# Kernel optimization log

Hardware: AMD Instinct MI355X
Metric: run time of the kernel (lower is better)

## Reference

```python
import jax, jax.numpy as jnp
import numpy as np

S, B, D = 4096, 4, 1024
APERTURE = 256
SCALE = 1.0 / np.sqrt(D)
EPS = 1e-6
NEG_INF = -jnp.inf


def _xavier(key, shape, gain=np.sqrt(2.0)):
    fan_in, fan_out = shape[1], shape[0]
    a = gain * np.sqrt(6.0 / (fan_in + fan_out))
    return jax.random.uniform(key, shape, jnp.float32, -a, a)


def setup_inputs() -> dict:
    key = jax.random.key(0)
    ks = jax.random.split(key, 8)
    return {
        "x": jax.random.normal(ks[0], (S, B, D), jnp.float32),
        "Wk": _xavier(ks[1], (D, D)),
        "Wq": _xavier(ks[2], (D, D)),
        "Wv": _xavier(ks[3], (D, D)),
        "Wp": _xavier(ks[4], (D, D)),
        "W1": _xavier(ks[5], (D, D)),
        "b1": jnp.full((D,), 0.1, jnp.float32),
        "W2": _xavier(ks[6], (1, D)),
        "b2": jnp.full((1,), 0.1, jnp.float32),
        "gamma": jnp.ones((D,), jnp.float32),
        "beta": jnp.zeros((D,), jnp.float32),
    }


def _layer_norm(y, gamma, beta):
    m = jnp.mean(y, axis=-1, keepdims=True)
    v = jnp.mean((y - m) ** 2, axis=-1, keepdims=True)
    return (y - m) * jax.lax.rsqrt(v + EPS) * gamma + beta


def reference(x, Wk, Wq, Wv, Wp, W1, b1, W2, b2, gamma, beta):
    # x: (S, B, D) -> (B, S, D)
    xb = jnp.transpose(x, (1, 0, 2))
    K = jnp.einsum('bsd,ed->bse', xb, Wk)
    Q = jnp.einsum('bsd,ed->bse', xb, Wq)
    V = jnp.einsum('bsd,ed->bse', xb, Wv)
    e = jnp.einsum('bqd,bkd->bqk', Q, K) * SCALE  # (B, S, S)
    # ignore_self: -inf on diagonal
    eye = jnp.eye(S, dtype=bool)
    e = jnp.where(eye[None, :, :], NEG_INF, e)
    # aperture mask: torch masks where tril(e,ap)*triu(e,-ap) == 0
    scope = jnp.tril(e, APERTURE) * jnp.triu(e, -APERTURE)
    e = jnp.where(scope == 0, NEG_INF, e)
    alpha = jax.nn.softmax(e, axis=2)  # dropout is identity at eval
    c = jnp.einsum('bqk,bkd->bqd', alpha, V)
    c = jnp.einsum('bqd,ed->bqe', c, Wp)
    y = c + xb
    y = _layer_norm(y, gamma, beta)
    y = jax.nn.relu(jnp.einsum('bsd,ed->bse', y, W1) + b1)
    y = _layer_norm(y, gamma, beta)
    y = jax.nn.sigmoid(jnp.einsum('bsd,ed->bse', y, W2) + b2)  # (B, S, 1)
    return jnp.transpose(y, (1, 0, 2))  # (S, B, 1)
```

## Files before the change

### kernel.cpp

```cpp
#include <hip/hip_runtime.h>
#include <stdint.h>
#include <math.h>

#define S_LEN 4096
#define BATCH 4
#define DIM   1024
#define AP    256
#define NBLK  32
#define BANDC 640
#define SCALE 0.03125f

typedef __attribute__((ext_vector_type(4))) float f32x4;
typedef __attribute__((ext_vector_type(8))) short bf16x8;

__device__ __forceinline__ ushort f2bf(float f) {
  union { float f; uint32_t u; } v; v.f = f;
  uint32_t r = v.u + 0x7FFFu + ((v.u >> 16) & 1u);
  return (ushort)(r >> 16);
}

__device__ __forceinline__ void gload16(const void* g, void* l) {
  __builtin_amdgcn_global_load_lds((const __attribute__((address_space(1))) void*)g,
                                   (__attribute__((address_space(3))) void*)l,
                                   16, 0, 0);
}

__device__ __forceinline__ float block_sum(float v, float* red) {
  #pragma unroll
  for (int o = 32; o > 0; o >>= 1) v += __shfl_xor(v, o, 64);
  const int w = threadIdx.x >> 6;
  if ((threadIdx.x & 63) == 0) red[w] = v;
  __syncthreads();
  v = red[0] + red[1] + red[2] + red[3];
  __syncthreads();
  return v;
}

__device__ __forceinline__ float block_max(float v, float* red) {
  #pragma unroll
  for (int o = 32; o > 0; o >>= 1) v = fmaxf(v, __shfl_xor(v, o, 64));
  const int w = threadIdx.x >> 6;
  if ((threadIdx.x & 63) == 0) red[w] = v;
  __syncthreads();
  v = fmaxf(fmaxf(red[0], red[1]), fmaxf(red[2], red[3]));
  __syncthreads();
  return v;
}

__device__ __forceinline__ void gemm256_core(
    const ushort* __restrict__ Ablk, int lda,
    const ushort* __restrict__ Bblk, int ldb,
    int K, ushort* __restrict__ lds,
    f32x4 acc[8][4])
{
  const int tid  = threadIdx.x;
  const int lane = tid & 63;
  const int wave = tid >> 6;
  const int wr = wave >> 2;
  const int wn = wave & 3;

  const int srow = tid >> 2;
  const int gseg = (tid & 3) ^ ((tid >> 3) & 3);
  const ushort* gA0 = Ablk + (size_t)srow * lda + gseg * 8;
  const ushort* gA1 = Ablk + (size_t)(srow + 128) * lda + gseg * 8;
  const ushort* gB0 = Bblk + (size_t)srow * ldb + gseg * 8;
  const ushort* gB1 = Bblk + (size_t)(srow + 128) * ldb + gseg * 8;
  const int stA = wave * 512;

  const int l15 = lane & 15;
  const int seg = (lane >> 4) ^ ((lane >> 1) & 3);
  const int roffA = (wr * 128 + l15) * 32 + seg * 8;
  const int roffB = (wn * 64  + l15) * 32 + seg * 8;

  const int NT = K >> 5;

  #pragma unroll
  for (int p = 0; p < 3; ++p) {
    ushort* buf = lds + p * 16384;
    const int k0 = p * 32;
    gload16(gA0 + k0, buf + stA);
    gload16(gA1 + k0, buf + 4096  + stA);
    gload16(gB0 + k0, buf + 8192  + stA);
    gload16(gB1 + k0, buf + 12288 + stA);
  }

  for (int t = 0; t < NT; ++t) {
    const int rem = NT - 1 - t;
    if (rem >= 2)      asm volatile("s_waitcnt vmcnt(8)" ::: "memory");
    else if (rem == 1) asm volatile("s_waitcnt vmcnt(4)" ::: "memory");
    else               asm volatile("s_waitcnt vmcnt(0)" ::: "memory");
    __builtin_amdgcn_s_barrier();

    if (t + 3 < NT) {
      ushort* buf = lds + ((t + 3) & 3) * 16384;
      const int k0 = (t + 3) * 32;
      gload16(gA0 + k0, buf + stA);
      gload16(gA1 + k0, buf + 4096  + stA);
      gload16(gB0 + k0, buf + 8192  + stA);
      gload16(gB1 + k0, buf + 12288 + stA);
    }

    const ushort* buf = lds + (t & 3) * 16384;
    bf16x8 af[4], af2[4], bfv[4];
    #pragma unroll
    for (int n = 0; n < 4; ++n) bfv[n] = *(const bf16x8*)(buf + 8192 + roffB + n * 512);
    #pragma unroll
    for (int m = 0; m < 4; ++m) af[m] = *(const bf16x8*)(buf + roffA + m * 512);
    #pragma unroll
    for (int m = 0; m < 4; ++m) af2[m] = *(const bf16x8*)(buf + roffA + (m + 4) * 512);

    __builtin_amdgcn_s_setprio(1);
    #pragma unroll
    for (int m = 0; m < 4; ++m)
      #pragma unroll
      for (int n = 0; n < 4; ++n)
        acc[m][n] = __builtin_amdgcn_mfma_f32_16x16x32_bf16(af[m], bfv[n], acc[m][n], 0, 0, 0);
    #pragma unroll
    for (int m = 0; m < 4; ++m)
      #pragma unroll
      for (int n = 0; n < 4; ++n)
        acc[m + 4][n] = __builtin_amdgcn_mfma_f32_16x16x32_bf16(af2[m], bfv[n], acc[m + 4][n], 0, 0, 0);
    __builtin_amdgcn_s_setprio(0);
    asm volatile("s_waitcnt lgkmcnt(0)" ::: "memory");
  }
}

#define ACC256_ZERO(acc) \
  _Pragma("unroll") for (int m_ = 0; m_ < 8; m_++) \
  _Pragma("unroll") for (int n_ = 0; n_ < 4; n_++) \
  _Pragma("unroll") for (int r_ = 0; r_ < 4; r_++) acc[m_][n_][r_] = 0.0f;

#define EPI256_BEGIN(acc) { \
  const int lane_ = threadIdx.x & 63; \
  const int wave_ = threadIdx.x >> 6; \
  const int wrb_ = (wave_ >> 2) * 128; \
  const int wnb_ = (wave_ & 3) * 64; \
  const int rb_ = (lane_ >> 4) << 2; \
  const int cb_ = lane_ & 15; \
  _Pragma("unroll") for (int m_ = 0; m_ < 8; m_++) \
  _Pragma("unroll") for (int n_ = 0; n_ < 4; n_++) \
  _Pragma("unroll") for (int r_ = 0; r_ < 4; r_++) { \
    const int rloc = wrb_ + m_ * 16 + rb_ + r_; \
    const int cloc = wnb_ + n_ * 16 + cb_; \
    const float aval = acc[m_][n_][r_];
#define EPI256_END() } }

__device__ __forceinline__ void gemm_core(
    const ushort* __restrict__ Ablk, int lda,
    const ushort* __restrict__ Bblk, int ldb,
    int k_begin, int k_end,
    ushort* __restrict__ lds,
    f32x4 acc[4][4])
{
  const int tid  = threadIdx.x;
  const int lane = tid & 63;
  const int wr = ((tid >> 7) & 1) * 64;
  const int wc = ((tid >> 6) & 1) * 64;
  const int lr = lane & 15;
  const int seg = (lane >> 4) ^ ((lane >> 1) & 3);

  const int srow = tid >> 2;
  const int gseg = (tid & 3) ^ ((tid >> 3) & 3);
  const ushort* gA0 = Ablk + (size_t)srow * lda + gseg * 8;
  const ushort* gA1 = Ablk + (size_t)(srow + 64) * lda + gseg * 8;
  const ushort* gB0 = Bblk + (size_t)srow * ldb + gseg * 8;
  const ushort* gB1 = Bblk + (size_t)(srow + 64) * ldb + gseg * 8;
  const int stA = (tid >> 6) * 512;

  const int NT = (k_end - k_begin) >> 5;

  gload16(gA0 + k_begin, lds + stA);
  gload16(gA1 + k_begin, lds + 2048 + stA);
  gload16(gB0 + k_begin, lds + 4096 + stA);
  gload16(gB1 + k_begin, lds + 6144 + stA);

  for (int t = 0; t < NT; ++t) {
    if (t + 1 < NT) {
      ushort* buf = lds + ((t + 1) & 1) * 8192;
      const int k0 = k_begin + (t + 1) * 32;
      gload16(gA0 + k0, buf + stA);
      gload16(gA1 + k0, buf + 2048 + stA);
      gload16(gB0 + k0, buf + 4096 + stA);
      gload16(gB1 + k0, buf + 6144 + stA);
      asm volatile("s_waitcnt vmcnt(4)" ::: "memory");
    } else {
      asm volatile("s_waitcnt vmcnt(0)" ::: "memory");
    }
    __builtin_amdgcn_s_barrier();

    const ushort* buf = lds + (t & 1) * 8192;
    bf16x8 af[4], bfv[4];
    #pragma unroll
    for (int m = 0; m < 4; m++)
      af[m] = *(const bf16x8*)(buf + (wr + m * 16 + lr) * 32 + seg * 8);
    #pragma unroll
    for (int n = 0; n < 4; n++)
      bfv[n] = *(const bf16x8*)(buf + 4096 + (wc + n * 16 + lr) * 32 + seg * 8);

    __builtin_amdgcn_s_setprio(1);
    #pragma unroll
    for (int m = 0; m < 4; m++)
      #pragma unroll
      for (int n = 0; n < 4; n++)
        acc[m][n] = __builtin_amdgcn_mfma_f32_16x16x32_bf16(af[m], bfv[n], acc[m][n], 0, 0, 0);
    __builtin_amdgcn_s_setprio(0);
    asm volatile("s_waitcnt lgkmcnt(0)" ::: "memory");
  }
}

#define ACC_ZERO(acc) \
  _Pragma("unroll") for (int m_ = 0; m_ < 4; m_++) \
  _Pragma("unroll") for (int n_ = 0; n_ < 4; n_++) \
  _Pragma("unroll") for (int r_ = 0; r_ < 4; r_++) acc[m_][n_][r_] = 0.0f;

#define EPI_BEGIN(acc) { \
  const int lane_ = threadIdx.x & 63; \
  const int wr_ = ((threadIdx.x >> 7) & 1) * 64; \
  const int wc_ = ((threadIdx.x >> 6) & 1) * 64; \
  const int rb_ = (lane_ >> 4) << 2; \
  const int cb_ = lane_ & 15; \
  _Pragma("unroll") for (int m_ = 0; m_ < 4; m_++) \
  _Pragma("unroll") for (int n_ = 0; n_ < 4; n_++) \
  _Pragma("unroll") for (int r_ = 0; r_ < 4; r_++) { \
    const int rloc = wr_ + m_ * 16 + rb_ + r_; \
    const int cloc = wc_ + n_ * 16 + cb_; \
    const float aval = acc[m_][n_][r_];
#define EPI_END() } }

__global__ __launch_bounds__(256) void prep_x(const float* __restrict__ x, ushort* __restrict__ xb) {
  size_t idx = ((size_t)blockIdx.x * 256 + threadIdx.x) * 4;
  int d = (int)(idx & 1023);
  int s = (int)((idx >> 10) & 4095);
  int b = (int)(idx >> 22);
  float4 v = *(const float4*)(x + ((size_t)s * BATCH + b) * DIM + d);
  ushort4 o;
  o.x = f2bf(v.x); o.y = f2bf(v.y); o.z = f2bf(v.z); o.w = f2bf(v.w);
  *(ushort4*)(xb + idx) = o;
}

__global__ __launch_bounds__(256) void f2bf_vec(const float* __restrict__ src, ushort* __restrict__ dst, int n) {
  int idx = (blockIdx.x * 256 + threadIdx.x) * 4;
  if (idx >= n) return;
  float4 v = *(const float4*)(src + idx);
  ushort4 o;
  o.x = f2bf(v.x); o.y = f2bf(v.y); o.z = f2bf(v.z); o.w = f2bf(v.w);
  *(ushort4*)(dst + idx) = o;
}

__global__ __launch_bounds__(512, 2) void qkv_gemm256(
    const ushort* __restrict__ xb, const ushort* __restrict__ wqkv,
    ushort* __restrict__ Kp, ushort* __restrict__ Qp, ushort* __restrict__ Vp)
{
  __shared__ ushort lds[65536];
  const int nid = (blockIdx.x & 7) * 96 + (blockIdx.x >> 3);
  const int by = nid / 12;
  const int bx = nid % 12;
  f32x4 acc[8][4];
  ACC256_ZERO(acc)
  gemm256_core(xb + (size_t)by * 256 * DIM, DIM,
               wqkv + (size_t)bx * 256 * DIM, DIM, DIM, lds, acc);
  ushort* dst = (bx < 4) ? Kp : (bx < 8) ? Qp : Vp;
  const int colb = (bx & 3) * 256;
  EPI256_BEGIN(acc)
    int row = by * 256 + rloc;
    int col = colb + cloc;
    dst[(size_t)row * DIM + col] = f2bf(aval);
  EPI256_END()
}

__global__ __launch_bounds__(512, 2) void wp_gemm256(
    const ushort* __restrict__ cbuf, const ushort* __restrict__ wpb,
    const float* __restrict__ x, float* __restrict__ y0)
{
  __shared__ ushort lds[65536];
  const int nid = (blockIdx.x & 7) * 32 + (blockIdx.x >> 3);
  const int by = nid >> 2;
  const int bx = nid & 3;
  f32x4 acc[8][4];
  ACC256_ZERO(acc)
  gemm256_core(cbuf + (size_t)by * 256 * DIM, DIM,
               wpb + (size_t)bx * 256 * DIM, DIM, DIM, lds, acc);
  EPI256_BEGIN(acc)
    int row = by * 256 + rloc;
    int col = bx * 256 + cloc;
    int b = row >> 12, s = row & 4095;
    y0[(size_t)row * DIM + col] = aval + x[((size_t)s * BATCH + b) * DIM + col];
  EPI256_END()
}

__global__ __launch_bounds__(512, 2) void ffn1_gemm256(
    const ushort* __restrict__ y1, const ushort* __restrict__ w1b,
    const float* __restrict__ b1, float* __restrict__ h0)
{
  __shared__ ushort lds[65536];
  const int nid = (blockIdx.x & 7) * 32 + (blockIdx.x >> 3);
  const int by = nid >> 2;
  const int bx = nid & 3;
  f32x4 acc[8][4];
  ACC256_ZERO(acc)
  gemm256_core(y1 + (size_t)by * 256 * DIM, DIM,
               w1b + (size_t)bx * 256 * DIM, DIM, DIM, lds, acc);
  EPI256_BEGIN(acc)
    int row = by * 256 + rloc;
    int col = bx * 256 + cloc;
    h0[(size_t)row * DIM + col] = fmaxf(aval + b1[col], 0.0f);
  EPI256_END()
}

__global__ __launch_bounds__(256) void transpose_v(const ushort* __restrict__ V, ushort* __restrict__ VT) {
  __shared__ ushort tile[64][66];
  const int s0 = blockIdx.x * 64, d0 = blockIdx.y * 64, b = blockIdx.z;
  const ushort* Vb = V + (size_t)b * S_LEN * DIM;
  ushort* VTb = VT + (size_t)b * DIM * S_LEN;
  #pragma unroll
  for (int it = 0; it < 16; it++) {
    int flat = it * 256 + threadIdx.x;
    int r = flat >> 6, c = flat & 63;
    tile[r][c] = Vb[(size_t)(s0 + r) * DIM + d0 + c];
  }
  __syncthreads();
  #pragma unroll
  for (int it = 0; it < 16; it++) {
    int flat = it * 256 + threadIdx.x;
    int r = flat >> 6, c = flat & 63;
    VTb[(size_t)(d0 + r) * S_LEN + s0 + c] = tile[c][r];
  }
}

__global__ __launch_bounds__(256) void scores_gemm(
    const ushort* __restrict__ Qp, const ushort* __restrict__ Kp,
    float* __restrict__ eband)
{
  const int nid = (blockIdx.x & 7) * 80 + (blockIdx.x >> 3);
  const int b   = nid / 160;
  const int rem = nid % 160;
  const int i   = rem / 5;
  const int jj  = rem % 5;
  const int j   = i - 2 + jj;
  if (j < 0 || j >= NBLK) return;
  __shared__ ushort lds[16384];
  f32x4 acc[4][4];
  ACC_ZERO(acc)
  gemm_core(Qp + ((size_t)b * S_LEN + i * 128) * DIM, DIM,
            Kp + ((size_t)b * S_LEN + j * 128) * DIM, DIM, 0, DIM, lds, acc);
  EPI_BEGIN(acc)
    int q = i * 128 + rloc;
    int k = j * 128 + cloc;
    float v = aval * SCALE;
    int dqk = q - k;
    if (dqk == 0 || dqk > AP || dqk < -AP) v = -INFINITY;
    eband[((size_t)b * S_LEN + q) * BANDC + jj * 128 + cloc] = v;
  EPI_END()
}

__global__ __launch_bounds__(256) void softmax_band(const float* __restrict__ eband,
                                                    ushort* __restrict__ aband)
{
  __shared__ float red[4];
  const int qg = blockIdx.x;
  const int s  = qg & 4095;
  const int i  = s >> 7;
  const float* row = eband + (size_t)qg * BANDC;
  ushort* arow = aband + (size_t)qg * BANDC;

  float vals[3];
  bool  valid[3];
  float mx = -INFINITY;
  #pragma unroll
  for (int t = 0; t < 3; t++) {
    int idx = threadIdx.x + t * 256;
    int jj = idx >> 7;
    int j = i - 2 + jj;
    bool ok = (idx < BANDC) && (j >= 0) && (j < NBLK);
    valid[t] = ok;
    float v = ok ? row[idx] : -INFINITY;
    vals[t] = v;
    mx = fmaxf(mx, v);
  }
  float bmax = block_max(mx, red);
  float ss = 0.0f;
  #pragma unroll
  for (int t = 0; t < 3; t++) {
    float e = valid[t] ? __expf(vals[t] - bmax) : 0.0f;
    vals[t] = e;
    ss += e;
  }
  float inv = 1.0f / block_sum(ss, red);
  #pragma unroll
  for (int t = 0; t < 3; t++) {
    int idx = threadIdx.x + t * 256;
    if (idx < BANDC) arow[idx] = f2bf(vals[t] * inv);
  }
}

__global__ __launch_bounds__(256) void av_gemm(
    const ushort* __restrict__ aband, const ushort* __restrict__ VT,
    ushort* __restrict__ cbuf)
{
  const int nid = (blockIdx.x & 7) * 128 + (blockIdx.x >> 3);
  const int by = nid >> 3;
  const int b = by >> 5, i = by & 31;
  const int bx = nid & 7;
  const int jj_lo = (i < 2) ? (2 - i) : 0;
  const int jj_hi = (i > 29) ? (34 - i) : 5;
  __shared__ ushort lds[16384];
  f32x4 acc[4][4];
  ACC_ZERO(acc)
  const ushort* Ablk = aband + ((size_t)b * S_LEN + i * 128) * BANDC;
  const ushort* Bblk = VT + (size_t)b * DIM * S_LEN + (size_t)bx * 128 * S_LEN + (i - 2) * 128;
  gemm_core(Ablk, BANDC, Bblk, S_LEN, jj_lo * 128, jj_hi * 128, lds, acc);
  EPI_BEGIN(acc)
    int row = b * S_LEN + i * 128 + rloc;
    int col = bx * 128 + cloc;
    cbuf[(size_t)row * DIM + col] = f2bf(aval);
  EPI_END()
}

__global__ __launch_bounds__(256) void ln_kernel(const float* __restrict__ y0, ushort* __restrict__ y1,
                                                 const float* __restrict__ gamma, const float* __restrict__ beta)
{
  __shared__ float red[4];
  const size_t q = blockIdx.x;
  const float* row = y0 + q * DIM;
  float v[4];
  #pragma unroll
  for (int t = 0; t < 4; t++) v[t] = row[threadIdx.x + t * 256];
  float mean = block_sum(v[0] + v[1] + v[2] + v[3], red) * (1.0f / DIM);
  float q2 = 0.0f;
  #pragma unroll
  for (int t = 0; t < 4; t++) { float d = v[t] - mean; q2 += d * d; }
  float var = block_sum(q2, red) * (1.0f / DIM);
  float rstd = rsqrtf(var + 1e-6f);
  #pragma unroll
  for (int t = 0; t < 4; t++) {
    int d = threadIdx.x + t * 256;
    y1[q * DIM + d] = f2bf((v[t] - mean) * rstd * gamma[d] + beta[d]);
  }
}

__global__ __launch_bounds__(256) void head_kernel(const float* __restrict__ h0,
    const float* __restrict__ gamma, const float* __restrict__ beta,
    const float* __restrict__ W2, const float* __restrict__ b2,
    float* __restrict__ out)
{
  __shared__ float red[4];
  const int qg = blockIdx.x;
  const int b = qg >> 12, s = qg & 4095;
  const float* row = h0 + (size_t)qg * DIM;
  float v[4];
  #pragma unroll
  for (int t = 0; t < 4; t++) v[t] = row[threadIdx.x + t * 256];
  float mean = block_sum(v[0] + v[1] + v[2] + v[3], red) * (1.0f / DIM);
  float q2 = 0.0f;
  #pragma unroll
  for (int t = 0; t < 4; t++) { float d = v[t] - mean; q2 += d * d; }
  float var = block_sum(q2, red) * (1.0f / DIM);
  float rstd = rsqrtf(var + 1e-6f);
  float part = 0.0f;
  #pragma unroll
  for (int t = 0; t < 4; t++) {
    int d = threadIdx.x + t * 256;
    part += ((v[t] - mean) * rstd * gamma[d] + beta[d]) * W2[d];
  }
  float logit = block_sum(part, red) + b2[0];
  if (threadIdx.x == 0) out[(size_t)s * BATCH + b] = 1.0f / (1.0f + expf(-logit));
}

extern "C" void kernel_launch(void* const* d_in, const int* in_sizes, int n_in,
                              void* d_out, int out_size, void* d_ws, size_t ws_size,
                              hipStream_t stream) {
  const float* x     = (const float*)d_in[0];
  const float* Wk    = (const float*)d_in[1];
  const float* Wq    = (const float*)d_in[2];
  const float* Wv    = (const float*)d_in[3];
  const float* Wp    = (const float*)d_in[4];
  const float* W1    = (const float*)d_in[5];
  const float* b1    = (const float*)d_in[6];
  const float* W2    = (const float*)d_in[7];
  const float* b2    = (const float*)d_in[8];
  const float* gamma = (const float*)d_in[9];
  const float* beta  = (const float*)d_in[10];
  float* out = (float*)d_out;

  char* w = (char*)d_ws;
  ushort* xb   = (ushort*)(w + 0);
  ushort* wqkv = (ushort*)(w + 33554432);
  ushort* wpb  = (ushort*)(w + 39845888);
  ushort* w1b  = (ushort*)(w + 41943040);
  ushort* Qp   = (ushort*)(w + 44040192);
  ushort* Kp   = (ushort*)(w + 77594624);
  ushort* Vp   = (ushort*)(w + 111149056);
  ushort* VT   = (ushort*)(w + 144703488);
  float*  big  = (float*)(w + 178257920);
  ushort* aband = Qp;
  ushort* cbuf  = Kp;
  ushort* y1    = Vp;
  float* eband = big;
  float* y0    = big;
  float* h0    = big;

  prep_x<<<16384, 256, 0, stream>>>(x, xb);
  f2bf_vec<<<1024, 256, 0, stream>>>(Wk, wqkv,            1048576);
  f2bf_vec<<<1024, 256, 0, stream>>>(Wq, wqkv + 1048576,  1048576);
  f2bf_vec<<<1024, 256, 0, stream>>>(Wv, wqkv + 2097152,  1048576);
  f2bf_vec<<<1024, 256, 0, stream>>>(Wp, wpb, 1048576);
  f2bf_vec<<<1024, 256, 0, stream>>>(W1, w1b, 1048576);

  qkv_gemm256<<<768, 512, 0, stream>>>(xb, wqkv, Kp, Qp, Vp);
  transpose_v<<<dim3(64, 16, 4), 256, 0, stream>>>(Vp, VT);
  scores_gemm<<<640, 256, 0, stream>>>(Qp, Kp, eband);
  softmax_band<<<16384, 256, 0, stream>>>(eband, aband);
  av_gemm<<<1024, 256, 0, stream>>>(aband, VT, cbuf);
  wp_gemm256<<<256, 512, 0, stream>>>(cbuf, wpb, x, y0);
  ln_kernel<<<16384, 256, 0, stream>>>(y0, y1, gamma, beta);
  ffn1_gemm256<<<256, 512, 0, stream>>>(y1, w1b, b1, h0);
  head_kernel<<<16384, 256, 0, stream>>>(h0, gamma, beta, W2, b2, out);
}
```

Before: 385.2 us.

## Restructure GEMM main loop into 4-phase ping-pong schedule with 64-wide K tiles

Replaces the 4-buffer, K=32 pipelined loop in the 256x256 GEMM core with a double-buffered, K=64-per-iteration loop. Each iteration is split into four phases, each pairing a subset of LDS fragment reads and global-to-LDS staging with a 16-MFMA quad. Phases are fenced by barriers, sched_barriers and setprio so memory traffic and MFMA work interleave more finely. This adds more barriers per iteration and depends on the vmcnt bookkeeping being correct across phases.

After: 383.4 us. No clear change (-0.5%).

```diff
diff --git a/kernel.cpp b/kernel.cpp
--- a/kernel.cpp
+++ b/kernel.cpp
@@ -47,6 +47,26 @@
   return v;
 }
 
+#define STAGE2(dstbase, g0, g1, kcol) \
+  gload16((g0) + (kcol), lds + (dstbase) + stOff); \
+  gload16((g1) + (kcol), lds + (dstbase) + 4096 + stOff);
+
+#define MFMA_QUAD(arow, bvec) \
+  _Pragma("unroll") for (int m = 0; m < 4; ++m) \
+  _Pragma("unroll") for (int n = 0; n < 4; ++n) \
+    acc[(arow) + m][n] = __builtin_amdgcn_mfma_f32_16x16x32_bf16(a[m], bvec[n], acc[(arow) + m][n], 0, 0, 0);
+
+#define PHASE_TAIL() \
+  __builtin_amdgcn_s_barrier(); \
+  asm volatile("s_waitcnt lgkmcnt(0)" ::: "memory"); \
+  __builtin_amdgcn_sched_barrier(0); \
+  __builtin_amdgcn_s_setprio(1);
+
+#define PHASE_END() \
+  __builtin_amdgcn_s_setprio(0); \
+  __builtin_amdgcn_sched_barrier(0); \
+  __builtin_amdgcn_s_barrier();
+
 __device__ __forceinline__ void gemm256_core(
     const ushort* __restrict__ Ablk, int lda,
     const ushort* __restrict__ Bblk, int ldb,
@@ -65,63 +85,69 @@
   const ushort* gA1 = Ablk + (size_t)(srow + 128) * lda + gseg * 8;
   const ushort* gB0 = Bblk + (size_t)srow * ldb + gseg * 8;
   const ushort* gB1 = Bblk + (size_t)(srow + 128) * ldb + gseg * 8;
-  const int stA = wave * 512;
+  const int stOff = wave * 512;
 
   const int l15 = lane & 15;
   const int seg = (lane >> 4) ^ ((lane >> 1) & 3);
-  const int roffA = (wr * 128 + l15) * 32 + seg * 8;
-  const int roffB = (wn * 64  + l15) * 32 + seg * 8;
-
-  const int NT = K >> 5;
-
-  #pragma unroll
-  for (int p = 0; p < 3; ++p) {
-    ushort* buf = lds + p * 16384;
-    const int k0 = p * 32;
-    gload16(gA0 + k0, buf + stA);
-    gload16(gA1 + k0, buf + 4096  + stA);
-    gload16(gB0 + k0, buf + 8192  + stA);
-    gload16(gB1 + k0, buf + 12288 + stA);
-  }
+  const int raBase = (wr * 128 + l15) * 32 + seg * 8;
+  const int rbBase = (wn * 64  + l15) * 32 + seg * 8;
+
+  const int NT = K >> 6;
+
+  STAGE2(0,     gA0, gA1, 0)
+  STAGE2(16384, gB0, gB1, 0)
+  STAGE2(8192,  gA0, gA1, 32)
+  STAGE2(24576, gB0, gB1, 32)
+  asm volatile("s_waitcnt vmcnt(4)" ::: "memory");
+  __builtin_amdgcn_s_barrier();
 
   for (int t = 0; t < NT; ++t) {
-    const int rem = NT - 1 - t;
-    if (rem >= 2)      asm volatile("s_waitcnt vmcnt(8)" ::: "memory");
-    else if (rem == 1) asm volatile("s_waitcnt vmcnt(4)" ::: "memory");
-    else               asm volatile("s_waitcnt vmcnt(0)" ::: "memory");
-    __builtin_amdgcn_s_barrier();
-
-    if (t + 3 < NT) {
-      ushort* buf = lds + ((t + 3) & 3) * 16384;
-      const int k0 = (t + 3) * 32;
-      gload16(gA0 + k0, buf + stA);
-      gload16(gA1 + k0, buf + 4096  + stA);
-      gload16(gB0 + k0, buf + 8192  + stA);
-      gload16(gB1 + k0, buf + 12288 + stA);
+    const int rb = (t & 1) * 32768;
+    const int sb = ((t + 1) & 1) * 32768;
+    const int k1 = (t + 1) << 6;
+    const bool more = (t + 1 < NT);
+
+    bf16x8 a[4], b0[4], b1[4];
+
+    #pragma unroll
+    for (int m = 0; m < 4; ++m) a[m] = *(const bf16x8*)(lds + rb + raBase + m * 512);
+    #pragma unroll
+    for (int n = 0; n < 4; ++n) b0[n] = *(const bf16x8*)(lds + rb + 16384 + rbBase + n * 512);
+    if (more) { STAGE2(sb, gA0, gA1, k1) }
+    PHASE_TAIL()
+    MFMA_QUAD(0, b0)
+    PHASE_END()
+
+    #pragma unroll
+    for (int m = 0; m < 4; ++m) a[m] = *(const bf16x8*)(lds + rb + raBase + (m + 4) * 512);
+    if (more) {
+      STAGE2(sb + 16384, gB0, gB1, k1)
+      asm volatile("s_waitcnt vmcnt(4)" ::: "memory");
+    } else {
+      asm volatile("s_waitcnt vmcnt(0)" ::: "memory");
     }
-
-    const ushort* buf = lds + (t & 3) * 16384;
-    bf16x8 af[4], af2[4], bfv[4];
-    #pragma unroll
-    for (int n = 0; n < 4; ++n) bfv[n] = *(const bf16x8*)(buf + 8192 + roffB + n * 512);
-    #pragma unroll
-    for (int m = 0; m < 4; ++m) af[m] = *(const bf16x8*)(buf + roffA + m * 512);
-    #pragma unroll
-    for (int m = 0; m < 4; ++m) af2[m] = *(const bf16x8*)(buf + roffA + (m + 4) * 512);
-
-    __builtin_amdgcn_s_setprio(1);
-    #pragma unroll
-    for (int m = 0; m < 4; ++m)
-      #pragma unroll
-      for (int n = 0; n < 4; ++n)
-        acc[m][n] = __builtin_amdgcn_mfma_f32_16x16x32_bf16(af[m], bfv[n], acc[m][n], 0, 0, 0);
-    #pragma unroll
-    for (int m = 0; m < 4; ++m)
-      #pragma unroll
-      for (int n = 0; n < 4; ++n)
-        acc[m + 4][n] = __builtin_amdgcn_mfma_f32_16x16x32_bf16(af2[m], bfv[n], acc[m + 4][n], 0, 0, 0);
-    __builtin_amdgcn_s_setprio(0);
-    asm volatile("s_waitcnt lgkmcnt(0)" ::: "memory");
+    PHASE_TAIL()
+    MFMA_QUAD(4, b0)
+    PHASE_END()
+
+    #pragma unroll
+    for (int m = 0; m < 4; ++m) a[m] = *(const bf16x8*)(lds + rb + 8192 + raBase + m * 512);
+    #pragma unroll
+    for (int n = 0; n < 4; ++n) b1[n] = *(const bf16x8*)(lds + rb + 24576 + rbBase + n * 512);
+    if (more) { STAGE2(sb + 8192, gA0, gA1, k1 + 32) }
+    PHASE_TAIL()
+    MFMA_QUAD(0, b1)
+    PHASE_END()
+
+    #pragma unroll
+    for (int m = 0; m < 4; ++m) a[m] = *(const bf16x8*)(lds + rb + 8192 + raBase + (m + 4) * 512);
+    if (more) {
+      STAGE2(sb + 24576, gB0, gB1, k1 + 32)
+      asm volatile("s_waitcnt vmcnt(4)" ::: "memory");
+    }
+    PHASE_TAIL()
+    MFMA_QUAD(4, b1)
+    PHASE_END()
   }
 }
 
```
